# Performance work log

Hardware: AMD Instinct MI355X
Metric: run time of the kernel (lower is better)

Reference implementation:

```python
import jax, jax.numpy as jnp
import numpy as np
from jax import lax

# SSD300/COCO geometry
B, P, C = 16, 8732, 81
V_CENTER, V_SIZE = 0.1, 0.2        # box coder variances
SCORE_THRESH = 0.05
NMS_THRESH = 0.45
DETS_PER_IMG = 100
PRE_NMS_TOPK = 1000                # fixed-size candidate set for jit-compatible NMS
MIN_SIZE = 0.01                    # remove_small_boxes threshold


def setup_inputs() -> dict:
    key = jax.random.key(0)
    k1, k2, k3, k4, k5 = jax.random.split(key, 5)
    # scale logits so a realistic fraction of softmax scores clears SCORE_THRESH
    pred_logits = jax.random.normal(k1, (B, P, C), jnp.float32) * 2.0
    pred_boxes = jax.random.normal(k2, (B, P, 4), jnp.float32) * 0.5
    # priors in (cx, cy, w, h), normalized coords, positive sizes
    cxcy = jax.random.uniform(k3, (P, 2), jnp.float32, 0.05, 0.95)
    wh = jax.random.uniform(k4, (P, 2), jnp.float32, 0.02, 0.4)
    priors = jnp.concatenate([cxcy, wh], axis=-1)
    target_sizes = jax.random.randint(k5, (B, 2), 480, 1333)  # (h, w) per image
    return {"pred_logits": pred_logits, "pred_boxes": pred_boxes,
            "priors": priors, "target_sizes": target_sizes}


def _decode(rel, priors):
    # SSD box coder: rel = (dx, dy, dw, dh), priors = (cx, cy, w, h) -> xyxy
    cxcy = priors[:, :2] + rel[:, :2] * V_CENTER * priors[:, 2:]
    wh = priors[:, 2:] * jnp.exp(rel[:, 2:] * V_SIZE)
    return jnp.concatenate([cxcy - 0.5 * wh, cxcy + 0.5 * wh], axis=-1)


def _pairwise_iou(b):
    # b: [K, 4] xyxy
    area = (b[:, 2] - b[:, 0]) * (b[:, 3] - b[:, 1])
    lt = jnp.maximum(b[:, None, :2], b[None, :, :2])
    rb = jnp.minimum(b[:, None, 2:], b[None, :, 2:])
    whi = jnp.clip(rb - lt, 0.0)
    inter = whi[..., 0] * whi[..., 1]
    return inter / (area[:, None] + area[None, :] - inter + 1e-9)


def _per_image(logits, rel, priors, size_hw):
    nc1 = C - 1  # foreground classes
    # decode and scale to pixel coords: target_size.flip(0).repeat(2) = [w, h, w, h]
    size_hw = size_hw.astype(jnp.float32)
    whwh = jnp.concatenate([size_hw[::-1], size_hw[::-1]])
    boxes = _decode(rel, priors) * whwh                     # [P, 4]
    scores = jax.nn.softmax(logits, axis=-1)[:, 1:]          # [P, C-1], drop background
    # score threshold + remove_small_boxes, fused as a mask (jit-safe)
    size_ok = ((boxes[:, 2] - boxes[:, 0]) >= MIN_SIZE) & \
              ((boxes[:, 3] - boxes[:, 1]) >= MIN_SIZE)      # [P]
    valid = (scores > SCORE_THRESH) & size_ok[:, None]       # [P, C-1]
    s_flat = jnp.where(valid, scores, -1.0).reshape(-1)      # [P*(C-1)]
    vals, idx = lax.top_k(s_flat, PRE_NMS_TOPK)
    prior_idx = idx // nc1
    labels_k = idx % nc1 + 1                                 # class ids in [1, C)
    boxes_k = boxes[prior_idx]                               # [K, 4]
    vmask = vals > 0.0                                       # real candidates
    # batched_nms via per-class coordinate offset
    max_coord = jnp.max(jnp.where(vmask[:, None], boxes_k, 0.0))
    offs_boxes = boxes_k + (labels_k.astype(jnp.float32) * (max_coord + 1.0))[:, None]
    iou = _pairwise_iou(offs_boxes)                          # [K, K]
    cols = jnp.arange(PRE_NMS_TOPK)

    def body(i, keep):
        suppress = (iou[i] > NMS_THRESH) & keep[i] & (cols > i)
        return keep & ~suppress

    keep = lax.fori_loop(0, PRE_NMS_TOPK, body, vmask)
    kept_scores = jnp.where(keep, vals, -1.0)
    fvals, fidx = lax.top_k(kept_scores, DETS_PER_IMG)
    fvalid = fvals > 0.0
    out_boxes = jnp.where(fvalid[:, None], boxes_k[fidx], 0.0)
    out_scores = jnp.where(fvalid, fvals, 0.0)
    out_labels = jnp.where(fvalid, labels_k[fidx], -1)
    return out_boxes, out_scores, out_labels


def reference(pred_logits, pred_boxes, priors, target_sizes):
    boxes, scores, labels = jax.vmap(_per_image, in_axes=(0, 0, None, 0))(
        pred_logits, pred_boxes, priors, target_sizes)
    # padded, fixed-size equivalent of the per-image list of dicts
    return boxes, scores, labels
```

## Files before the change

kernel.cpp:

```cpp
#include <hip/hip_runtime.h>
#include <math.h>

#pragma clang fp contract(off)

#define NIMG 16
#define NP   8732
#define NCLS 81
#define NFG  80
#define KTOP 1000
#define KPAD 1024
#define DETS 100
#define CAPMAX 166912
#define BASEBITS 0x3D000000u
#define CNT_STRIDE 64
#define TILEB 137
#define NBIN 1280

#define OFF_BOXES  0u
#define OFF_CNT    2235392u
#define OFF_SCNT   2239488u
#define OFF_GHIST  2243584u
#define OFF_SBUF   2325504u
#define OFF_T      2587648u
#define OFF_CSCORE 2591744u
#define OFF_CLABEL 2657280u
#define OFF_CBOX   2722816u
#define OFF_COFFS  2984960u
#define OFF_CAREA  3247104u
#define OFF_VALIDW 3312640u
#define OFF_MASK   3314688u
#define OFF_CAND   5411840u
#define MEMSET_LEN 90112u

typedef unsigned long long u64;
typedef unsigned int u32;

#define AS_GLOBAL __attribute__((address_space(1)))
#define AS_LOCAL  __attribute__((address_space(3)))

__global__ __launch_bounds__(256, 6) void k_decode(
    const float* __restrict__ logits, const float* __restrict__ rel,
    const float* __restrict__ priors, const int* __restrict__ tsz,
    float* __restrict__ boxes_out, u64* __restrict__ cand,
    u32* __restrict__ cnt, int cap)
{
#pragma clang fp contract(off)
    __shared__ __align__(16) float lx[64 * NCLS];
    __shared__ float pmx[4 * 64];
    __shared__ float psm[4 * 64];
    __shared__ u32 sok[64];
    __shared__ u32 wtt[4];
    __shared__ u32 sbase;
    int b  = blockIdx.x / TILEB;
    int g  = blockIdx.x - b * TILEB;
    int p0 = g * 64;
    int t  = threadIdx.x;
    int lane = t & 63;
    int q = t >> 6;
    int npri = NP - p0; if (npri > 64) npri = 64;
    int words = npri * NCLS;

    const u32* s32 = (const u32*)(logits + ((size_t)b * NP + p0) * NCLS);
    u32* lxw = (u32*)lx;
    int full = words >> 8;
    for (int k = q; k < full; k += 4)
        __builtin_amdgcn_global_load_lds(
            (AS_GLOBAL const u32*)(s32 + (k << 8) + (lane << 2)),
            (AS_LOCAL u32*)(lxw + (k << 8)), 16, 0, 0);
    int base = full << 8;
    int c4 = (words - base) >> 6;
    for (int k = q; k < c4; k += 4)
        __builtin_amdgcn_global_load_lds(
            (AS_GLOBAL const u32*)(s32 + base + (k << 6) + lane),
            (AS_LOCAL u32*)(lxw + base + (k << 6)), 4, 0, 0);
    int base2 = base + (c4 << 6);
    if (q == 0 && lane < words - base2) lxw[base2 + lane] = s32[base2 + lane];

    int p = p0 + lane;
    bool active = p < NP;

    if (q == 0) {
        u32 ok = 0;
        if (active) {
            float4 pr = ((const float4*)priors)[p];
            float4 rl = ((const float4*)rel)[(size_t)b * NP + p];
            float W = (float)tsz[b * 2 + 1], H = (float)tsz[b * 2 + 0];
            float cx = pr.x + (rl.x * 0.1f) * pr.z;
            float cy = pr.y + (rl.y * 0.1f) * pr.w;
            float w_ = pr.z * expf(rl.z * 0.2f);
            float h_ = pr.w * expf(rl.w * 0.2f);
            float4 bx;
            bx.x = (cx - 0.5f * w_) * W; bx.y = (cy - 0.5f * h_) * H;
            bx.z = (cx + 0.5f * w_) * W; bx.w = (cy + 0.5f * h_) * H;
            ((float4*)boxes_out)[(size_t)b * NP + p] = bx;
            ok = ((bx.z - bx.x) >= 0.01f) && ((bx.w - bx.y) >= 0.01f);
        }
        sok[lane] = ok;
    }
    __syncthreads();

    int tb = lane * NCLS;
    int nk = (q == 0) ? 21 : 20;
    float x[21];
    #pragma unroll
    for (int k = 0; k < 21; ++k) {
        int c = q + 4 * k;
        x[k] = (k < nk) ? lx[tb + c] : -3.4e38f;
    }
    float pm = -3.4e38f;
    #pragma unroll
    for (int k = 0; k < 21; ++k) if (k < nk) pm = fmaxf(pm, x[k]);
    pmx[q * 64 + lane] = pm;
    __syncthreads();
    float m = fmaxf(fmaxf(pmx[lane], pmx[64 + lane]),
                    fmaxf(pmx[128 + lane], pmx[192 + lane]));

    float ps = 0.f;
    #pragma unroll
    for (int k = 0; k < 21; ++k) {
        if (k < nk) { x[k] = expf(x[k] - m); ps += x[k]; }
    }
    psm[q * 64 + lane] = ps;
    __syncthreads();
    float s = (psm[lane] + psm[64 + lane]) + (psm[128 + lane] + psm[192 + lane]);

    float hi = 0.05000075f * s;
    float lo = 0.04999925f * s;
    u32 pass = 0, band = 0;
    u32 sizeok = sok[lane];
    if (active && sizeok) {
        #pragma unroll
        for (int k = 0; k < 21; ++k) {
            int c = q + 4 * k;
            if (k < nk && c >= 1) {
                bool pa = x[k] > hi;
                bool bd = (!pa) && (x[k] > lo);
                pass |= ((u32)pa) << k;
                band |= ((u32)bd) << k;
            }
        }
    }
    while (band) {
        int k = __builtin_ctz(band); band &= band - 1;
        int c = q + 4 * k;
        float e = expf(lx[tb + c] - m);
        if (e / s > 0.05f) pass |= 1u << k;
    }
    int cnt_t = __popc(pass);

    int pre = cnt_t;
    #pragma unroll
    for (int d = 1; d < 64; d <<= 1) {
        int o = __shfl_up(pre, d);
        if (lane >= d) pre += o;
    }
    if (lane == 63) wtt[q] = (u32)pre;
    __syncthreads();
    u32 before = 0;
    for (int w = 0; w < 4; ++w) if (w < q) before += wtt[w];
    if (t == 0) {
        u32 tot = wtt[0] + wtt[1] + wtt[2] + wtt[3];
        sbase = tot ? atomicAdd(cnt + b * CNT_STRIDE, tot) : 0u;
    }
    __syncthreads();
    u32 pos = sbase + before + (u32)(pre - cnt_t);

    u64* cb = cand + (size_t)b * cap;
    u32 flatneg = 0xFFFFFFFFu - (u32)p * NFG;
    while (pass) {
        int k = __builtin_ctz(pass); pass &= pass - 1;
        int c = q + 4 * k;
        float e = expf(lx[tb + c] - m);
        float d = e / s;
        if ((int)pos < cap)
            cb[pos] = ((u64)__float_as_uint(d) << 32) | (u64)(flatneg - (u32)(c - 1));
        ++pos;
    }
}

__global__ __launch_bounds__(256) void k_hist(
    const u64* __restrict__ cand, const u32* __restrict__ cnt,
    u32* __restrict__ ghist, int cap)
{
    __shared__ u32 h[NBIN];
    int b = blockIdx.x >> 4, sl = blockIdx.x & 15;
    int t = threadIdx.x;
    for (int i = t; i < NBIN; i += 256) h[i] = 0;
    u32 n = min(cnt[b * CNT_STRIDE], (u32)cap);
    __syncthreads();
    const u64* cb = cand + (size_t)b * cap;
    u32 lo = (u32)(((u64)n * (u32)sl) >> 4);
    u32 hi = (u32)(((u64)n * (u32)(sl + 1)) >> 4);
    for (u32 i = lo + (u32)t; i < hi; i += 256) {
        u32 sb = (u32)(cb[i] >> 32);
        u32 bin = (sb - BASEBITS) >> 15;
        if (bin > NBIN - 1) bin = NBIN - 1;
        atomicAdd(&h[bin], 1u);
    }
    __syncthreads();
    for (int i = t; i < NBIN; i += 256)
        if (h[i]) atomicAdd(ghist + b * NBIN + i, h[i]);
}

__device__ __forceinline__ void suffix_find(
    u32* hist, u32* wt, u32 K, int tid,
    volatile int* outI, volatile u32* outNext)
{
    int lane = tid & 63, w = tid >> 6;
    u32 v[8]; u32 tot = 0;
    #pragma unroll
    for (int k = 0; k < 8; ++k) { v[k] = hist[tid * 8 + k]; tot += v[k]; }
    u32 ws = tot;
    #pragma unroll
    for (int d = 1; d < 64; d <<= 1) {
        u32 o = __shfl_down(ws, d);
        if (lane + d < 64) ws += o;
    }
    if (lane == 0) wt[w] = ws;
    __syncthreads();
    u32 tail = 0;
    for (int w2 = w + 1; w2 < 16; ++w2) tail += wt[w2];
    u32 after = (ws - tot) + tail;
    u32 sufk[9];
    sufk[8] = after;
    #pragma unroll
    for (int k = 7; k >= 0; --k) sufk[k] = v[k] + sufk[k + 1];
    #pragma unroll
    for (int k = 0; k < 8; ++k) {
        if (sufk[k] >= K && sufk[k + 1] < K) {
            *outI = tid * 8 + k;
            *outNext = sufk[k + 1];
        }
    }
    __syncthreads();
}

__global__ __launch_bounds__(1024) void k_findc(
    const u32* __restrict__ ghist, const u64* __restrict__ cand,
    const u32* __restrict__ cnt, u32* __restrict__ Tarr, int cap)
{
    __shared__ u32 h[NBIN];
    __shared__ u32 fh[8192];
    __shared__ u32 wt[16];
    __shared__ int sh_c, sh_i2;
    __shared__ u32 sh_S, sh_next, sh_d;
    int b = blockIdx.x, t = threadIdx.x;
    for (int i = t; i < NBIN; i += 1024) h[i] = ghist[b * NBIN + i];
    if (t == 0) { sh_c = -2; sh_i2 = -2; sh_S = 0; sh_next = 0; }
    __syncthreads();
    if (t < 64) {
        u32 v[20]; u32 tot = 0;
        #pragma unroll
        for (int k = 0; k < 20; ++k) { v[k] = h[t * 20 + k]; tot += v[k]; }
        u32 ws = tot;
        #pragma unroll
        for (int d = 1; d < 64; d <<= 1) {
            u32 o = (u32)__shfl_down((int)ws, d);
            if (t + d < 64) ws += o;
        }
        u32 suf[21];
        suf[20] = ws - tot;
        #pragma unroll
        for (int k = 19; k >= 0; --k) suf[k] = v[k] + suf[k + 1];
        #pragma unroll
        for (int k = 0; k < 20; ++k) {
            if (suf[k] >= (u32)KTOP && suf[k + 1] < (u32)KTOP) {
                sh_c = t * 20 + k; sh_S = suf[k]; sh_next = suf[k + 1];
            }
        }
    }
    __syncthreads();
    int c = sh_c;
    u32 T = 0;
    if (c >= 0) {
        if (sh_S <= 2048u) {
            T = BASEBITS + ((u32)c << 15);
        } else {
            u32 nhi = sh_next;
            for (int i = t; i < 8192; i += 1024) fh[i] = 0;
            __syncthreads();
            u32 n = min(cnt[b * CNT_STRIDE], (u32)cap);
            const u64* cb = cand + (size_t)b * cap;
            for (u32 i = (u32)t; i < n; i += 1024) {
                u32 sb = (u32)(cb[i] >> 32);
                if ((int)((sb - BASEBITS) >> 15) == c)
                    atomicAdd(&fh[(sb >> 2) & 0x1FFFu], 1u);
            }
            __syncthreads();
            suffix_find(fh, wt, (u32)KTOP - nhi, t, &sh_i2, &sh_d);
            T = (sh_i2 >= 0) ? (BASEBITS + ((u32)c << 15) + ((u32)sh_i2 << 2))
                             : (BASEBITS + ((u32)c << 15));
        }
    }
    if (t == 0) Tarr[b * CNT_STRIDE] = T;
}

__global__ __launch_bounds__(256) void k_compact(
    const u64* __restrict__ cand, const u32* __restrict__ cnt,
    const u32* __restrict__ Tarr, u64* __restrict__ sbuf,
    u32* __restrict__ scnt, int cap)
{
    int b = blockIdx.x >> 4, sl = blockIdx.x & 15;
    int tid = threadIdx.x, lane = tid & 63;
    u32 n = min(cnt[b * CNT_STRIDE], (u32)cap);
    u32 T = Tarr[b * CNT_STRIDE];
    const u64* cb = cand + (size_t)b * cap;
    u64* sb = sbuf + b * 2048;
    u32 lo = (u32)(((u64)n * (u32)sl) >> 4);
    u32 hi = (u32)(((u64)n * (u32)(sl + 1)) >> 4);
    for (u32 basei = lo; basei < hi; basei += 256) {
        u32 i = basei + (u32)tid;
        u64 key = (i < hi) ? cb[i] : 0ULL;
        bool pick = (i < hi) && ((u32)(key >> 32) >= T);
        u64 bal = __ballot(pick);
        u32 wb = 0;
        if (lane == 0 && bal) wb = atomicAdd(scnt + b * CNT_STRIDE, (u32)__popcll(bal));
        wb = (u32)__shfl((int)wb, 0);
        if (pick) {
            u32 pos = wb + (u32)__popcll(bal & ((1ULL << lane) - 1ULL));
            if (pos < 2048) sb[pos] = key;
        }
    }
}

__global__ __launch_bounds__(1024) void k_sort(
    const u64* __restrict__ sbuf, const u32* __restrict__ scnt,
    const float* __restrict__ boxes,
    float* __restrict__ cscore, int* __restrict__ clabel,
    float4* __restrict__ cbox, float4* __restrict__ coffs,
    float* __restrict__ carea, u64* __restrict__ validw)
{
#pragma clang fp contract(off)
    __shared__ u64 buf[2048];
    __shared__ float red[1024];
    int b = blockIdx.x, tid = threadIdx.x;
    int lane = tid & 63;
    u32 m = min(scnt[b * CNT_STRIDE], 2048u);
    int size = (m > 1024u) ? 2048 : 1024;
    const u64* sb = sbuf + b * 2048;
    for (int i = tid; i < size; i += 1024) buf[i] = ((u32)i < m) ? sb[i] : 0ULL;
    __syncthreads();
    for (int k = 2; k <= size; k <<= 1) {
        for (int j = k >> 1; j > 0; j >>= 1) {
            for (int i = tid; i < size; i += 1024) {
                int ixj = i ^ j;
                if (ixj > i) {
                    u64 a = buf[i], bb = buf[ixj];
                    bool up = (i & k) == 0;
                    if (up ? (a < bb) : (a > bb)) { buf[i] = bb; buf[ixj] = a; }
                }
            }
            __syncthreads();
        }
    }
    u64 key = (tid < KTOP) ? buf[tid] : 0ULL;
    float s = __uint_as_float((u32)(key >> 32));
    bool valid = s > 0.0f;
    u32 flat = valid ? (0xFFFFFFFFu - (u32)key) : 0u;
    int prior = (int)(flat / NFG);
    int cls = (int)(flat - (u32)prior * NFG) + 1;
    float4 bx = make_float4(0.f, 0.f, 0.f, 0.f);
    if (valid) bx = ((const float4*)boxes)[b * NP + prior];
    cscore[b * KPAD + tid] = s;
    clabel[b * KPAD + tid] = cls;
    cbox[b * KPAD + tid] = bx;
    u64 vb = __ballot(valid);
    if (lane == 0) validw[b * 16 + (tid >> 6)] = vb;
    float lm = valid ? fmaxf(fmaxf(bx.x, bx.y), fmaxf(bx.z, bx.w)) : 0.0f;
    red[tid] = fmaxf(lm, 0.0f);
    __syncthreads();
    for (int d = 512; d > 0; d >>= 1) {
        if (tid < d) red[tid] = fmaxf(red[tid], red[tid + d]);
        __syncthreads();
    }
    float mc = red[0];
    float off = (float)cls * (mc + 1.0f);
    float4 ob = valid ? make_float4(bx.x + off, bx.y + off, bx.z + off, bx.w + off)
                      : make_float4(0.f, 0.f, 0.f, 0.f);
    float area = valid ? (ob.z - ob.x) * (ob.w - ob.y) : 0.0f;
    coffs[b * KPAD + tid] = ob;
    carea[b * KPAD + tid] = area;
}

__global__ __launch_bounds__(1024) void k_iou(
    const float4* __restrict__ coffs, const float* __restrict__ carea,
    u64* __restrict__ cmask)
{
#pragma clang fp contract(off)
    __shared__ float4 bs[KPAD];
    __shared__ float as_[KPAD];
    int b = blockIdx.x >> 4, tile = blockIdx.x & 15;
    int t = threadIdx.x;
    bs[t] = coffs[b * KPAD + t];
    as_[t] = carea[b * KPAD + t];
    __syncthreads();
    int j = tile * 64 + (t & 63);
    int w = t >> 6;
    float4 bj = bs[j];
    float aj = as_[j];
    int r0 = w * 64;
    u64 bits = 0;
    #pragma unroll 4
    for (int k = 0; k < 64; ++k) {
        int r = r0 + k;
        float4 br = bs[r];
        float ar = as_[r];
        float ltx = fmaxf(br.x, bj.x), lty = fmaxf(br.y, bj.y);
        float rbx = fminf(br.z, bj.z), rby = fminf(br.w, bj.w);
        float wx = fmaxf(rbx - ltx, 0.0f), wy = fmaxf(rby - lty, 0.0f);
        float inter = wx * wy;
        float denom = ((ar + aj) - inter) + 1e-9f;
        float iou = inter / denom;
        bool sup = (iou > 0.45f) && (j > r);
        bits |= ((u64)sup) << k;
    }
    cmask[((size_t)b * 16 + w) * KPAD + j] = bits;
}

__global__ __launch_bounds__(64) void k_nms(
    const u64* __restrict__ cmask, const u64* __restrict__ validw,
    const float* __restrict__ cscore, const int* __restrict__ clabel,
    const float4* __restrict__ cbox, float* __restrict__ out)
{
    int b = blockIdx.x, lane = threadIdx.x;
    const u64* cm = cmask + (size_t)b * 16 * KPAD;
    u64 kept[16];
    u64 cw[16];
    #pragma unroll
    for (int w = 0; w < 16; ++w) cw[w] = cm[w * KPAD + lane];
    #pragma unroll
    for (int g = 0; g < 16; ++g) {
        u64 vg = validw[b * 16 + g];
        bool rem = false;
        #pragma unroll
        for (int w = 0; w < 16; ++w)
            if (w < g) rem |= (kept[w] & cw[w]) != 0ULL;
        u64 cg = cw[g];
        bool myv = ((vg >> lane) & 1ULL) && !rem;
        if (g < 15) {
            int cbase = (g + 1) * 64 + lane;
            #pragma unroll
            for (int w = 0; w < 16; ++w) cw[w] = cm[w * KPAD + cbase];
        }
        u64 K = __ballot(myv);
        for (;;) {
            u64 K2 = __ballot(myv && ((K & cg) == 0ULL));
            if (K2 == K) break;
            K = K2;
        }
        kept[g] = K;
    }
    __shared__ u64 sk[16];
    __shared__ int pfx[17];
    __shared__ int slot[DETS];
    if (lane == 0) {
        #pragma unroll
        for (int w = 0; w < 16; ++w) sk[w] = kept[w];
        int run = 0;
        #pragma unroll
        for (int l = 0; l < 16; ++l) { pfx[l] = run; run += __popcll(kept[l]); }
        pfx[16] = run;
    }
    __syncthreads();
    if (lane < 16) {
        int r = pfx[lane];
        u64 wv = sk[lane];
        while (wv && r < DETS) {
            int bit = __builtin_ctzll(wv);
            slot[r] = lane * 64 + bit;
            ++r;
            wv &= wv - 1;
        }
    }
    __syncthreads();
    int total = min(pfx[16], DETS);
    for (int r = lane; r < DETS; r += 64) {
        float4 bx = make_float4(0.f, 0.f, 0.f, 0.f);
        float s = 0.0f;
        int lb = -1;
        if (r < total) {
            int cdx = slot[r];
            bx = cbox[b * KPAD + cdx];
            s = cscore[b * KPAD + cdx];
            lb = clabel[b * KPAD + cdx];
        }
        float* ob = out + ((size_t)b * DETS + r) * 4;
        ob[0] = bx.x; ob[1] = bx.y; ob[2] = bx.z; ob[3] = bx.w;
        out[NIMG * DETS * 4 + b * DETS + r] = s;
        out[NIMG * DETS * 4 + NIMG * DETS + b * DETS + r] = (float)lb;
    }
}

extern "C" void kernel_launch(void* const* d_in, const int* in_sizes, int n_in,
                              void* d_out, int out_size, void* d_ws, size_t ws_size,
                              hipStream_t stream) {
    const float* logits = (const float*)d_in[0];
    const float* rel    = (const float*)d_in[1];
    const float* priors = (const float*)d_in[2];
    const int*   tsz    = (const int*)d_in[3];
    float* out = (float*)d_out;
    char* ws = (char*)d_ws;

    float* boxes  = (float*)(ws + OFF_BOXES);
    u32*   cnt    = (u32*)(ws + OFF_CNT);
    u32*   scnt   = (u32*)(ws + OFF_SCNT);
    u32*   ghist  = (u32*)(ws + OFF_GHIST);
    u64*   sbuf   = (u64*)(ws + OFF_SBUF);
    u32*   Tarr   = (u32*)(ws + OFF_T);
    float* cscore = (float*)(ws + OFF_CSCORE);
    int*   clabel = (int*)(ws + OFF_CLABEL);
    float4* cbox  = (float4*)(ws + OFF_CBOX);
    float4* coffs = (float4*)(ws + OFF_COFFS);
    float* carea  = (float*)(ws + OFF_CAREA);
    u64*   validw = (u64*)(ws + OFF_VALIDW);
    u64*   cmask  = (u64*)(ws + OFF_MASK);
    u64*   cand   = (u64*)(ws + OFF_CAND);

    long long avail = ((long long)ws_size - (long long)OFF_CAND) / (NIMG * 8);
    int cap = (int)(avail < CAPMAX ? (avail > 0 ? avail : 1) : CAPMAX);
    cap &= ~1;

    hipMemsetAsync(cnt, 0, MEMSET_LEN, stream);
    k_decode<<<NIMG * TILEB, 256, 0, stream>>>(logits, rel, priors, tsz,
                                               boxes, cand, cnt, cap);
    k_hist<<<NIMG * 16, 256, 0, stream>>>(cand, cnt, ghist, cap);
    k_findc<<<NIMG, 1024, 0, stream>>>(ghist, cand, cnt, Tarr, cap);
    k_compact<<<NIMG * 16, 256, 0, stream>>>(cand, cnt, Tarr, sbuf, scnt, cap);
    k_sort<<<NIMG, 1024, 0, stream>>>(sbuf, scnt, boxes, cscore, clabel,
                                      cbox, coffs, carea, validw);
    k_iou<<<NIMG * 16, 1024, 0, stream>>>(coffs, carea, cmask);
    k_nms<<<NIMG, 64, 0, stream>>>(cmask, validw, cscore, clabel, cbox, out);
}
```

Baseline: 160.4 us.

## Fuse histogram, threshold, compaction and sort into one per-image kernel

Replaces four kernels (histogram, threshold find, compaction, bitonic sort) with a single per-image kernel that builds the histogram in shared memory, finds the threshold, compacts directly into shared memory and sorts. This removes three launches, the global histogram and staging buffers, and their memset. In exchange, each image's candidate list (about 10k entries or more) is now scanned by a single 1024-thread block, up to three times, instead of 16 blocks per image, which reduces parallelism to 16 workgroups.

```diff
diff --git a/kernel.cpp b/kernel.cpp
--- a/kernel.cpp
+++ b/kernel.cpp
@@ -18,19 +18,14 @@
 
 #define OFF_BOXES  0u
 #define OFF_CNT    2235392u
-#define OFF_SCNT   2239488u
-#define OFF_GHIST  2243584u
-#define OFF_SBUF   2325504u
-#define OFF_T      2587648u
-#define OFF_CSCORE 2591744u
-#define OFF_CLABEL 2657280u
-#define OFF_CBOX   2722816u
-#define OFF_COFFS  2984960u
-#define OFF_CAREA  3247104u
-#define OFF_VALIDW 3312640u
-#define OFF_MASK   3314688u
-#define OFF_CAND   5411840u
-#define MEMSET_LEN 90112u
+#define OFF_CSCORE 2239488u
+#define OFF_CLABEL 2305024u
+#define OFF_CBOX   2370560u
+#define OFF_COFFS  2632704u
+#define OFF_CAREA  2894848u
+#define OFF_VALIDW 2960384u
+#define OFF_MASK   2962432u
+#define OFF_CAND   5059584u
 
 typedef unsigned long long u64;
 typedef unsigned int u32;
@@ -178,30 +173,6 @@
     }
 }
 
-__global__ __launch_bounds__(256) void k_hist(
-    const u64* __restrict__ cand, const u32* __restrict__ cnt,
-    u32* __restrict__ ghist, int cap)
-{
-    __shared__ u32 h[NBIN];
-    int b = blockIdx.x >> 4, sl = blockIdx.x & 15;
-    int t = threadIdx.x;
-    for (int i = t; i < NBIN; i += 256) h[i] = 0;
-    u32 n = min(cnt[b * CNT_STRIDE], (u32)cap);
-    __syncthreads();
-    const u64* cb = cand + (size_t)b * cap;
-    u32 lo = (u32)(((u64)n * (u32)sl) >> 4);
-    u32 hi = (u32)(((u64)n * (u32)(sl + 1)) >> 4);
-    for (u32 i = lo + (u32)t; i < hi; i += 256) {
-        u32 sb = (u32)(cb[i] >> 32);
-        u32 bin = (sb - BASEBITS) >> 15;
-        if (bin > NBIN - 1) bin = NBIN - 1;
-        atomicAdd(&h[bin], 1u);
-    }
-    __syncthreads();
-    for (int i = t; i < NBIN; i += 256)
-        if (h[i]) atomicAdd(ghist + b * NBIN + i, h[i]);
-}
-
 __device__ __forceinline__ void suffix_find(
     u32* hist, u32* wt, u32 K, int tid,
     volatile int* outI, volatile u32* outNext)
@@ -235,18 +206,41 @@
     __syncthreads();
 }
 
-__global__ __launch_bounds__(1024) void k_findc(
-    const u32* __restrict__ ghist, const u64* __restrict__ cand,
-    const u32* __restrict__ cnt, u32* __restrict__ Tarr, int cap)
+__global__ __launch_bounds__(1024) void k_select(
+    const u64* __restrict__ cand, const u32* __restrict__ cnt,
+    const float* __restrict__ boxes,
+    float* __restrict__ cscore, int* __restrict__ clabel,
+    float4* __restrict__ cbox, float4* __restrict__ coffs,
+    float* __restrict__ carea, u64* __restrict__ validw, int cap)
 {
+#pragma clang fp contract(off)
     __shared__ u32 h[NBIN];
     __shared__ u32 fh[8192];
     __shared__ u32 wt[16];
+    __shared__ u64 buf[2048];
+    __shared__ float red[1024];
     __shared__ int sh_c, sh_i2;
-    __shared__ u32 sh_S, sh_next, sh_d;
-    int b = blockIdx.x, t = threadIdx.x;
-    for (int i = t; i < NBIN; i += 1024) h[i] = ghist[b * NBIN + i];
-    if (t == 0) { sh_c = -2; sh_i2 = -2; sh_S = 0; sh_next = 0; }
+    __shared__ u32 sh_S, sh_next, sh_d, sh_m;
+    int b = blockIdx.x, t = threadIdx.x, lane = t & 63;
+    u32 n = min(cnt[b * CNT_STRIDE], (u32)cap);
+    const u64* cb = cand + (size_t)b * cap;
+
+    for (int i = t; i < NBIN; i += 1024) h[i] = 0;
+    if (t == 0) { sh_c = -2; sh_i2 = -2; sh_S = 0; sh_next = 0; sh_m = 0; }
+    __syncthreads();
+    if (t == 0 && (n & 1)) {
+        u32 sb = (u32)(cb[n - 1] >> 32);
+        u32 bin = (sb - BASEBITS) >> 15; if (bin > NBIN - 1) bin = NBIN - 1;
+        atomicAdd(&h[bin], 1u);
+    }
+    u32 npair = n >> 1;
+    for (u32 i = t; i < npair; i += 1024) {
+        uint4 v = ((const uint4*)cb)[i];
+        u32 b1 = (v.y - BASEBITS) >> 15; if (b1 > NBIN - 1) b1 = NBIN - 1;
+        u32 b2 = (v.w - BASEBITS) >> 15; if (b2 > NBIN - 1) b2 = NBIN - 1;
+        atomicAdd(&h[b1], 1u);
+        atomicAdd(&h[b2], 1u);
+    }
     __syncthreads();
     if (t < 64) {
         u32 v[20]; u32 tot = 0;
@@ -279,8 +273,6 @@
             u32 nhi = sh_next;
             for (int i = t; i < 8192; i += 1024) fh[i] = 0;
             __syncthreads();
-            u32 n = min(cnt[b * CNT_STRIDE], (u32)cap);
-            const u64* cb = cand + (size_t)b * cap;
             for (u32 i = (u32)t; i < n; i += 1024) {
                 u32 sb = (u32)(cb[i] >> 32);
                 if ((int)((sb - BASEBITS) >> 15) == c)
@@ -292,57 +284,27 @@
                              : (BASEBITS + ((u32)c << 15));
         }
     }
-    if (t == 0) Tarr[b * CNT_STRIDE] = T;
-}
-
-__global__ __launch_bounds__(256) void k_compact(
-    const u64* __restrict__ cand, const u32* __restrict__ cnt,
-    const u32* __restrict__ Tarr, u64* __restrict__ sbuf,
-    u32* __restrict__ scnt, int cap)
-{
-    int b = blockIdx.x >> 4, sl = blockIdx.x & 15;
-    int tid = threadIdx.x, lane = tid & 63;
-    u32 n = min(cnt[b * CNT_STRIDE], (u32)cap);
-    u32 T = Tarr[b * CNT_STRIDE];
-    const u64* cb = cand + (size_t)b * cap;
-    u64* sb = sbuf + b * 2048;
-    u32 lo = (u32)(((u64)n * (u32)sl) >> 4);
-    u32 hi = (u32)(((u64)n * (u32)(sl + 1)) >> 4);
-    for (u32 basei = lo; basei < hi; basei += 256) {
-        u32 i = basei + (u32)tid;
-        u64 key = (i < hi) ? cb[i] : 0ULL;
-        bool pick = (i < hi) && ((u32)(key >> 32) >= T);
+    u32 nr = (n + 63) & ~63u;
+    for (u32 i = t; i < nr; i += 1024) {
+        u64 key = (i < n) ? cb[i] : 0ULL;
+        bool pick = (i < n) && ((u32)(key >> 32) >= T);
         u64 bal = __ballot(pick);
         u32 wb = 0;
-        if (lane == 0 && bal) wb = atomicAdd(scnt + b * CNT_STRIDE, (u32)__popcll(bal));
+        if (lane == 0 && bal) wb = atomicAdd(&sh_m, (u32)__popcll(bal));
         wb = (u32)__shfl((int)wb, 0);
         if (pick) {
             u32 pos = wb + (u32)__popcll(bal & ((1ULL << lane) - 1ULL));
-            if (pos < 2048) sb[pos] = key;
-        }
-    }
-}
-
-__global__ __launch_bounds__(1024) void k_sort(
-    const u64* __restrict__ sbuf, const u32* __restrict__ scnt,
-    const float* __restrict__ boxes,
-    float* __restrict__ cscore, int* __restrict__ clabel,
-    float4* __restrict__ cbox, float4* __restrict__ coffs,
-    float* __restrict__ carea, u64* __restrict__ validw)
-{
-#pragma clang fp contract(off)
-    __shared__ u64 buf[2048];
-    __shared__ float red[1024];
-    int b = blockIdx.x, tid = threadIdx.x;
-    int lane = tid & 63;
-    u32 m = min(scnt[b * CNT_STRIDE], 2048u);
+            if (pos < 2048) buf[pos] = key;
+        }
+    }
+    __syncthreads();
+    u32 m = min(sh_m, 2048u);
     int size = (m > 1024u) ? 2048 : 1024;
-    const u64* sb = sbuf + b * 2048;
-    for (int i = tid; i < size; i += 1024) buf[i] = ((u32)i < m) ? sb[i] : 0ULL;
+    for (int i = t; i < size; i += 1024) if ((u32)i >= m) buf[i] = 0ULL;
     __syncthreads();
     for (int k = 2; k <= size; k <<= 1) {
         for (int j = k >> 1; j > 0; j >>= 1) {
-            for (int i = tid; i < size; i += 1024) {
+            for (int i = t; i < size; i += 1024) {
                 int ixj = i ^ j;
                 if (ixj > i) {
                     u64 a = buf[i], bb = buf[ixj];
@@ -353,7 +315,7 @@
             __syncthreads();
         }
     }
-    u64 key = (tid < KTOP) ? buf[tid] : 0ULL;
+    u64 key = (t < KTOP) ? buf[t] : 0ULL;
     float s = __uint_as_float((u32)(key >> 32));
     bool valid = s > 0.0f;
     u32 flat = valid ? (0xFFFFFFFFu - (u32)key) : 0u;
@@ -361,16 +323,16 @@
     int cls = (int)(flat - (u32)prior * NFG) + 1;
     float4 bx = make_float4(0.f, 0.f, 0.f, 0.f);
     if (valid) bx = ((const float4*)boxes)[b * NP + prior];
-    cscore[b * KPAD + tid] = s;
-    clabel[b * KPAD + tid] = cls;
-    cbox[b * KPAD + tid] = bx;
+    cscore[b * KPAD + t] = s;
+    clabel[b * KPAD + t] = cls;
+    cbox[b * KPAD + t] = bx;
     u64 vb = __ballot(valid);
-    if (lane == 0) validw[b * 16 + (tid >> 6)] = vb;
+    if (lane == 0) validw[b * 16 + (t >> 6)] = vb;
     float lm = valid ? fmaxf(fmaxf(bx.x, bx.y), fmaxf(bx.z, bx.w)) : 0.0f;
-    red[tid] = fmaxf(lm, 0.0f);
+    red[t] = fmaxf(lm, 0.0f);
     __syncthreads();
     for (int d = 512; d > 0; d >>= 1) {
-        if (tid < d) red[tid] = fmaxf(red[tid], red[tid + d]);
+        if (t < d) red[t] = fmaxf(red[t], red[t + d]);
         __syncthreads();
     }
     float mc = red[0];
@@ -378,8 +340,8 @@
     float4 ob = valid ? make_float4(bx.x + off, bx.y + off, bx.z + off, bx.w + off)
                       : make_float4(0.f, 0.f, 0.f, 0.f);
     float area = valid ? (ob.z - ob.x) * (ob.w - ob.y) : 0.0f;
-    coffs[b * KPAD + tid] = ob;
-    carea[b * KPAD + tid] = area;
+    coffs[b * KPAD + t] = ob;
+    carea[b * KPAD + t] = area;
 }
 
 __global__ __launch_bounds__(1024) void k_iou(
@@ -503,10 +465,6 @@
 
     float* boxes  = (float*)(ws + OFF_BOXES);
     u32*   cnt    = (u32*)(ws + OFF_CNT);
-    u32*   scnt   = (u32*)(ws + OFF_SCNT);
-    u32*   ghist  = (u32*)(ws + OFF_GHIST);
-    u64*   sbuf   = (u64*)(ws + OFF_SBUF);
-    u32*   Tarr   = (u32*)(ws + OFF_T);
     float* cscore = (float*)(ws + OFF_CSCORE);
     int*   clabel = (int*)(ws + OFF_CLABEL);
     float4* cbox  = (float4*)(ws + OFF_CBOX);
@@ -520,14 +478,11 @@
     int cap = (int)(avail < CAPMAX ? (avail > 0 ? avail : 1) : CAPMAX);
     cap &= ~1;
 
-    hipMemsetAsync(cnt, 0, MEMSET_LEN, stream);
+    hipMemsetAsync(cnt, 0, NIMG * CNT_STRIDE * 4, stream);
     k_decode<<<NIMG * TILEB, 256, 0, stream>>>(logits, rel, priors, tsz,
                                                boxes, cand, cnt, cap);
-    k_hist<<<NIMG * 16, 256, 0, stream>>>(cand, cnt, ghist, cap);
-    k_findc<<<NIMG, 1024, 0, stream>>>(ghist, cand, cnt, Tarr, cap);
-    k_compact<<<NIMG * 16, 256, 0, stream>>>(cand, cnt, Tarr, sbuf, scnt, cap);
-    k_sort<<<NIMG, 1024, 0, stream>>>(sbuf, scnt, boxes, cscore, clabel,
-                                      cbox, coffs, carea, validw);
+    k_select<<<NIMG, 1024, 0, stream>>>(cand, cnt, boxes, cscore, clabel,
+                                        cbox, coffs, carea, validw, cap);
     k_iou<<<NIMG * 16, 1024, 0, stream>>>(coffs, carea, cmask);
     k_nms<<<NIMG, 64, 0, stream>>>(cmask, validw, cscore, clabel, cbox, out);
 }
```

Measured after the change: 160.8 us. About the same (+0.3%).
